# Performance work log

Measured on AMD Instinct MI355X. Metric: run time of the kernel, lower is better.

## Reference

```python
import jax, jax.numpy as jnp
import numpy as np

NUM_ANCHORS = 32
MAX_DIST = 3
DDE_ROUNDS = 2
DDE_REV_ROUNDS = 2
PE_ANCHOR_DIM = 16


def setup_inputs() -> dict:
    key = jax.random.key(0)
    ks = jax.random.split(key, 20)
    N, Ntext, NT, E, R, D, H = 20000, 19500, 500, 200000, 500, 256, 256
    PE = DDE_ROUNDS + DDE_REV_ROUNDS + PE_ANCHOR_DIM + 3
    s = 0.02
    return {
        "h_ids": jax.random.randint(ks[0], (E,), 0, N),
        "r_ids": jax.random.randint(ks[1], (E,), 0, R),
        "t_ids": jax.random.randint(ks[2], (E,), 0, N),
        "q_emb": jax.random.normal(ks[3], (D,), jnp.float32),
        "entity_embs": jax.random.normal(ks[4], (Ntext, D), jnp.float32),
        "relation_embs": jax.random.normal(ks[5], (R, D), jnp.float32),
        "topic_entity_ids": jax.random.randint(ks[6], (4,), 0, N),
        "num_entities": N,
        "num_non_text_entities": NT,
        "non_text_emb": jax.random.normal(ks[7], (1, D)) * s,
        "dist_emb": jax.random.normal(ks[8], (MAX_DIST + 2, PE_ANCHOR_DIM)) * s,
        "W_enc": jax.random.normal(ks[9], (D + PE, H)) * s,
        "b_enc": jnp.zeros((H,)),
        "gnn_W_msg": jax.random.normal(ks[10], (2, H + D, H)) * s,
        "gnn_W_gate": jax.random.normal(ks[11], (2, 2 * H, H)) * s,
        "gnn_W_upd": jax.random.normal(ks[12], (2, H, H)) * s,
        "W_out": jax.random.normal(ks[13], (H, D)) * s,
        "scorer_W1": jax.random.normal(ks[14], (4 * D + 4, H)) * s,
        "scorer_b1": jnp.zeros((H,)),
        "scorer_W2": jax.random.normal(ks[15], (H, 1)) * s,
        "scorer_b2": jnp.zeros((1,)),
    }


def reference(h_ids, r_ids, t_ids, q_emb, entity_embs, relation_embs,
              topic_entity_ids, num_entities, num_non_text_entities,
              non_text_emb, dist_emb, W_enc, b_enc,
              gnn_W_msg, gnn_W_gate, gnn_W_upd, W_out,
              scorer_W1, scorer_b1, scorer_W2, scorer_b2):
    N = num_entities
    D = q_emb.shape[0]
    E = h_ids.shape[0]
    # assemble all entity embeddings (text + broadcast non-text)
    all_emb = jnp.concatenate(
        [entity_embs, jnp.broadcast_to(non_text_emb, (num_non_text_entities, D))], axis=0)
    # anchor triple selection: question-conditioned triple scores, top-k
    qe = all_emb @ q_emb            # [N]
    qr = relation_embs @ q_emb      # [R]
    tri_score = qe[h_ids] + qr[r_ids] + qe[t_ids]  # [E]
    anchor_scores, anchor_idx = jax.lax.top_k(tri_score, NUM_ANCHORS)
    # topic DDE positional encoding (mean-aggregated label propagation)
    topic = jnp.zeros((N,), all_emb.dtype).at[topic_entity_ids].set(1.0)
    deg_t = jnp.maximum(jnp.zeros((N,)).at[t_ids].add(1.0), 1.0)
    deg_h = jnp.maximum(jnp.zeros((N,)).at[h_ids].add(1.0), 1.0)
    cols = []
    s = topic
    for _ in range(DDE_ROUNDS):
        s = jnp.zeros((N,)).at[t_ids].add(s[h_ids]) / deg_t
        cols.append(s)
    s = topic
    for _ in range(DDE_REV_ROUNDS):
        s = jnp.zeros((N,)).at[h_ids].add(s[t_ids]) / deg_h
        cols.append(s)
    pe_topic = jnp.stack(cols, axis=1)  # [N, 4]
    # anchor proximity PE: bounded BFS distance, embedded
    anchor_mask = (jnp.zeros((N,)).at[h_ids[anchor_idx]].set(1.0)
                   .at[t_ids[anchor_idx]].set(1.0))
    FAR = float(MAX_DIST + 1)
    dist = jnp.where(anchor_mask > 0, 0.0, FAR)
    for _ in range(MAX_DIST):
        c1 = jnp.full((N,), FAR).at[t_ids].min(dist[h_ids] + 1.0)
        c2 = jnp.full((N,), FAR).at[h_ids].min(dist[t_ids] + 1.0)
        dist = jnp.minimum(dist, jnp.minimum(c1, c2))
    pe_anchor = dist_emb[dist.astype(jnp.int32)]  # [N, 16]
    # path indicators (topic flag, anchor-endpoint flag, subgraph mask = full graph)
    path_ind = jnp.stack([topic, anchor_mask, jnp.ones((N,))], axis=1)
    pe_full = jnp.concatenate([pe_topic, pe_anchor, path_ind], axis=1)  # [N, 23]
    # gated GNN refine over the (full) anchor subgraph
    h = jax.nn.relu(jnp.concatenate([all_emb, pe_full], axis=1) @ W_enc + b_enc)
    rel_e = relation_embs[r_ids]  # [E, D]
    for l in range(gnn_W_msg.shape[0]):
        msg = jax.nn.relu(jnp.concatenate([h[h_ids], rel_e], axis=1) @ gnn_W_msg[l])
        agg = jnp.zeros_like(h).at[t_ids].add(msg)
        gate = jax.nn.sigmoid(jnp.concatenate([h, agg], axis=1) @ gnn_W_gate[l])
        h = h + gate * jnp.tanh(agg @ gnn_W_upd[l])
    h_final = h @ W_out  # back to emb_dim, assembled over all entities
    # scalar triple features
    is_anchor = jnp.zeros((E,)).at[anchor_idx].set(1.0)
    a_score = jnp.zeros((E,)).at[anchor_idx].set(jax.lax.stop_gradient(anchor_scores))
    scalar_feats = jnp.stack([is_anchor, a_score, topic[h_ids], topic[t_ids]], axis=1)
    # triple scorer MLP
    feats = jnp.concatenate([
        jnp.broadcast_to(q_emb, (E, D)), h_final[h_ids], rel_e,
        h_final[t_ids], scalar_feats], axis=1)  # [E, 4D+4]
    hid = jax.nn.relu(feats @ scorer_W1 + scorer_b1)
    return (hid @ scorer_W2 + scorer_b2)[:, 0]
```

## Files before the change

### kernel.cpp

```cpp
#include <hip/hip_runtime.h>
#include <math.h>

#define CDIV(a,b) (((a)+(b)-1)/(b))

typedef short short8 __attribute__((ext_vector_type(8)));
typedef float f32x4  __attribute__((ext_vector_type(4)));
typedef unsigned short u16;

__device__ __forceinline__ float warp_sum(float v){
  #pragma unroll
  for (int o=32;o;o>>=1) v += __shfl_down(v,o);
  return v;
}
__device__ __forceinline__ int warp_min(int v){
  #pragma unroll
  for (int o=32;o;o>>=1) v = min(v,__shfl_down(v,o));
  return v;
}
__device__ __forceinline__ u16 f2bf(float f){
  unsigned u = __float_as_uint(f);
  unsigned r = 0x7fffu + ((u>>16)&1u);
  return (u16)((u + r)>>16);
}
__device__ __forceinline__ float bl(u16 v){ return __uint_as_float(((unsigned)v)<<16); }

__global__ __launch_bounds__(256)
void k_rowdot_all(const float* __restrict__ ent, const float* __restrict__ nontext,
                  const float* __restrict__ q, float* __restrict__ qe,
                  int N, int Ntext,
                  const float* __restrict__ rel, float* __restrict__ qr, int R, int nb1){
  int wid = threadIdx.x>>6, lane = threadIdx.x&63;
  const float* src; float* dst; int row;
  if ((int)blockIdx.x < nb1){
    row = blockIdx.x*4 + wid; if (row >= N) return;
    src = (row < Ntext) ? (ent + (size_t)row*256) : nontext;
    dst = qe;
  } else {
    row = (blockIdx.x-nb1)*4 + wid; if (row >= R) return;
    src = rel + (size_t)row*256;
    dst = qr;
  }
  float4 a = *(const float4*)(src + lane*4);
  float4 b = *(const float4*)(q + lane*4);
  float s = a.x*b.x + a.y*b.y + a.z*b.z + a.w*b.w;
  s = warp_sum(s);
  if (!lane) dst[row] = s;
}

__global__ __launch_bounds__(256)
void k_tri(const int* __restrict__ h, const int* __restrict__ r,
           const int* __restrict__ t, const float* __restrict__ qe,
           const float* __restrict__ qr, float* __restrict__ tri,
           float* __restrict__ bmax, int* __restrict__ degh, int* __restrict__ degi, int E){
  __shared__ float red[256];
  int e = blockIdx.x*256 + threadIdx.x;
  float v = -INFINITY;
  if (e < E){
    int hh=h[e], rr=r[e], tt=t[e];
    v = qe[hh] + qr[rr] + qe[tt];
    tri[e] = v;
    atomicAdd(&degh[hh], 1);
    atomicAdd(&degi[tt], 1);
  }
  red[threadIdx.x]=v; __syncthreads();
  for (int s=128;s;s>>=1){ if ((int)threadIdx.x<s) red[threadIdx.x]=fmaxf(red[threadIdx.x],red[threadIdx.x+s]); __syncthreads(); }
  if (!threadIdx.x) bmax[blockIdx.x]=red[0];
}

__global__ __launch_bounds__(64)
void k_thresh(const float* __restrict__ bmax, float* __restrict__ thrT, int nb){
  int lane = threadIdx.x;
  float m = -INFINITY;
  for (int i=lane; i<nb; i+=64) m = fmaxf(m, bmax[i]);
  for (int it=0; it<32; it++){
    float bv = m; int bln = lane;
    #pragma unroll
    for (int o=32;o;o>>=1){
      float ov = __shfl_down(bv,o);
      int   ol = __shfl_down(bln,o);
      if (ov>bv){ bv=ov; bln=ol; }
    }
    float mv = __shfl(bv,0);
    int   wl = __shfl(bln,0);
    if (lane==wl) m = -INFINITY;
    if (it==31 && lane==0) thrT[0]=mv;
  }
}

__global__ void k_compact(const float* __restrict__ tri, const float* __restrict__ thrT,
                          int* __restrict__ cnt, int* __restrict__ ci, float* __restrict__ cv, int E){
  int e = blockIdx.x*256 + threadIdx.x; if (e>=E) return;
  float v = tri[e];
  if (v >= thrT[0]){
    int p = atomicAdd(cnt, 1);
    ci[p]=e; cv[p]=v;
  }
}

__global__ __launch_bounds__(64)
void k_final32(const int* __restrict__ ci, const float* __restrict__ cv, const int* __restrict__ cnt,
               int* __restrict__ ai, float* __restrict__ as,
               const int* __restrict__ h_ids, const int* __restrict__ t_ids,
               const int* __restrict__ topicId, int nTopic,
               float* __restrict__ topic, float* __restrict__ amask){
  int lane = threadIdx.x;
  int C = *cnt; if (C > 1024) C = 1024;
  int nIter = CDIV(C,64);
  unsigned selMask = 0;
  int myai=0; float myas=0.f;
  for (int it=0; it<32; it++){
    float bv=-INFINITY; int bi=0x7fffffff; int bj=-1;
    for (int j=0;j<nIter;j++){
      int p = lane + j*64;
      if (p < C && !((selMask>>j)&1u)){
        float v = cv[p]; int idx = ci[p];
        if (v>bv || (v==bv && idx<bi)){ bv=v; bi=idx; bj=j; }
      }
    }
    int bln = lane;
    #pragma unroll
    for (int o=32;o;o>>=1){
      float ov=__shfl_down(bv,o); int oi=__shfl_down(bi,o);
      int   oj=__shfl_down(bj,o); int ol=__shfl_down(bln,o);
      if (ov>bv || (ov==bv && oi<bi)){ bv=ov; bi=oi; bj=oj; bln=ol; }
    }
    float wv=__shfl(bv,0); int wi=__shfl(bi,0);
    int   wj=__shfl(bj,0); int wl=__shfl(bln,0);
    if (lane==wl) selMask |= (1u<<wj);
    if (lane==it){ myai=wi; myas=wv; }
  }
  if (lane<32){
    ai[lane]=myai; as[lane]=myas;
    int e = myai;
    amask[h_ids[e]]=1.f;
    amask[t_ids[e]]=1.f;
  }
  if (lane<nTopic) topic[topicId[lane]]=1.f;
}

__global__ void k_scan1(const int* __restrict__ degT, const int* __restrict__ degH,
                        int* __restrict__ offsT, int* __restrict__ offsH,
                        int* __restrict__ bsum, int N, int nb){
  __shared__ int s[256];
  int which = (int)blockIdx.x >= nb;
  int b = which ? blockIdx.x - nb : blockIdx.x;
  const int* deg = which ? degH : degT;
  int* offs = which ? offsH : offsT;
  int i = b*256 + threadIdx.x;
  int v = (i<N) ? deg[i] : 0;
  s[threadIdx.x] = v; __syncthreads();
  #pragma unroll
  for (int o=1;o<256;o<<=1){
    int add = (threadIdx.x>=(unsigned)o) ? s[threadIdx.x-o] : 0; __syncthreads();
    s[threadIdx.x] += add; __syncthreads();
  }
  if (i<N) offs[i] = s[threadIdx.x] - v;
  if (threadIdx.x==255) bsum[blockIdx.x] = s[255];
}
__global__ void k_scan2two(int* __restrict__ bsum, int nb){
  __shared__ int s[256];
  int t=threadIdx.x;
  int half = t>>7, idx = t&127;
  int v = (idx<nb)? bsum[half*nb+idx] : 0;
  s[t]=v; __syncthreads();
  #pragma unroll
  for (int o=1;o<128;o<<=1){ int add=(idx>=o)?s[t-o]:0; __syncthreads(); s[t]+=add; __syncthreads(); }
  if (idx<nb) bsum[half*nb+idx] = s[t]-v;
}
__global__ void k_scan3(int* __restrict__ offsT, int* __restrict__ offsH,
                        const int* __restrict__ bsum,
                        int* __restrict__ curT, int* __restrict__ curH, int N, int nb){
  int which = (int)blockIdx.x >= nb;
  int b = which ? blockIdx.x - nb : blockIdx.x;
  int i = b*256+threadIdx.x; if (i>=N) return;
  int* offs = which ? offsH : offsT;
  int* cur  = which ? curH  : curT;
  int o = offs[i] + bsum[blockIdx.x];
  offs[i]=o; cur[i]=o;
}
__global__ void k_place(const int* __restrict__ h, const int* __restrict__ r,
                        const int* __restrict__ t,
                        int* __restrict__ curT, int* __restrict__ curH,
                        int4* __restrict__ ehr4, int* __restrict__ etH, int E){
  int e = blockIdx.x*256+threadIdx.x; if (e>=E) return;
  int hh=h[e], tt=t[e];
  int pos = atomicAdd(&curT[tt], 1);
  ehr4[pos] = make_int4(hh, r[e], e, 0);
  int posh = atomicAdd(&curH[hh], 1);
  etH[posh] = tt;
}

__global__ __launch_bounds__(256)
void k_dde2(const int* __restrict__ offsT, const int* __restrict__ degT, const int4* __restrict__ ehr4,
            const int* __restrict__ offsH, const int* __restrict__ degH, const int* __restrict__ etH,
            const float* __restrict__ s0, const float* __restrict__ s1,
            float* __restrict__ sn0, float* __restrict__ sn1,
            float* __restrict__ pe4, int c0, int c1,
            const float* __restrict__ amask, int* __restrict__ dist0, int N){
  int wid=threadIdx.x>>6, lane=threadIdx.x&63;
  int i = blockIdx.x*4+wid; if (i>=N) return;
  int dir = blockIdx.y;
  const int* offs = dir ? offsH : offsT;
  const int* deg  = dir ? degH  : degT;
  const float* s  = dir ? s1 : s0;
  float* sn       = dir ? sn1 : sn0;
  int col         = dir ? c1 : c0;
  int start=offs[i], cnt=deg[i];
  float a=0.f;
  if (dir){
    for (int k=lane;k<cnt;k+=64) a += s[etH[start+k]];
  } else {
    for (int k=lane;k<cnt;k+=64) a += s[ehr4[start+k].x];
  }
  a = warp_sum(a);
  if (!lane){
    float v = a / fmaxf((float)cnt,1.f);
    if (sn) sn[i]=v;
    pe4[i*4+col]=v;
    if (dist0 && !dir) dist0[i] = (amask[i]>0.f)?0:4;
  }
}

__global__ __launch_bounds__(256)
void k_bfs_g(const int* __restrict__ offsT, const int* __restrict__ degT, const int4* __restrict__ ehr4,
             const int* __restrict__ offsH, const int* __restrict__ degH, const int* __restrict__ etH,
             const int* __restrict__ din, int* __restrict__ dout, int N){
  int wid=threadIdx.x>>6, lane=threadIdx.x&63;
  int i = blockIdx.x*4+wid; if (i>=N) return;
  int sT=offsT[i], cT=degT[i];
  int sH=offsH[i], cH=degH[i];
  int best = 4;
  for (int k=lane;k<cT;k+=64) best = min(best, din[ehr4[sT+k].x]+1);
  for (int k=lane;k<cH;k+=64) best = min(best, din[etH[sH+k]]+1);
  best = warp_min(best);
  if (!lane) dout[i] = min(din[i], best);
}

__global__ void k_smalls(const float* __restrict__ dist_e, const float* __restrict__ W_enc,
                         float* __restrict__ distW,
                         const float* __restrict__ nontext, float* __restrict__ encnt,
                         const float* __restrict__ q, const float* __restrict__ W1,
                         const float* __restrict__ b1, float* __restrict__ bias2){
  int b = blockIdx.x, j = threadIdx.x;
  if (b < 5){
    const float* Wpe = W_enc + (256+4)*256;
    float s=0.f;
    #pragma unroll
    for (int p=0;p<16;p++) s += dist_e[b*16+p]*Wpe[p*256+j];
    distW[b*256+j]=s;
  } else if (b == 5){
    float s=0.f;
    for (int k=0;k<256;k++) s += nontext[k]*W_enc[k*256+j];
    encnt[j]=s;
  } else {
    float s=b1[j];
    for (int k=0;k<256;k++) s += q[k]*W1[k*256+j];
    bias2[j]=s;
  }
}

__global__ __launch_bounds__(64)
void k_packall(const float* __restrict__ W_enc, const float* __restrict__ W_msg,
               const float* __restrict__ W_gate, const float* __restrict__ W_upd,
               const float* __restrict__ W1, u16* __restrict__ pbAll){
  int f = blockIdx.x, lane = threadIdx.x;
  int tgt, fid, nt16;
  if      (f < 128) { tgt=0; fid=f;      nt16=16; }
  else if (f < 256) { tgt=1; fid=f-128;  nt16=16; }
  else if (f < 384) { tgt=2; fid=f-256;  nt16=16; }
  else if (f < 896) { tgt=3; fid=f-384;  nt16=32; }
  else if (f < 1408){ tgt=4; fid=f-896;  nt16=32; }
  else if (f < 1792){ tgt=5; fid=f-1408; nt16=48; }
  else              { tgt=6; fid=f-1792; nt16=32; }
  int ks = fid/nt16, nt = fid%nt16;
  int kb = ks*32 + 8*(lane>>4);
  int n  = nt*16 + (lane&15);
  u16 v[8];
  #pragma unroll
  for (int i=0;i<8;i++){
    int k = kb+i;
    float x;
    if (tgt==0) x = W_enc[(size_t)k*256+n];
    else if (tgt==1) x = W_msg[(size_t)k*256+n];
    else if (tgt==2) x = W_msg[(size_t)(512+k)*256+n];
    else if (tgt==3 || tgt==4){
      const float* Wg = W_gate + (tgt==4 ? (size_t)512*256 : 0);
      const float* Wu = W_upd  + (tgt==4 ? (size_t)256*256 : 0);
      int blk = n>>4, c = ((blk>>1)<<4) | (n&15);
      if ((blk&1)==0) x = Wg[(size_t)k*256+c];
      else            x = (k<256) ? 0.f : Wu[(size_t)(k-256)*256+c];
    }
    else if (tgt==5){
      if (n<256)      x = W_msg[(size_t)(256+k)*256+n];
      else if (n<512) x = W_msg[(size_t)(768+k)*256+(n-256)];
      else            x = W1[(size_t)(512+k)*256+(n-512)];
    } else {
      if (n<256) x = W1[(size_t)(256+k)*256+n];
      else       x = W1[(size_t)(768+k)*256+(n-256)];
    }
    v[i]=f2bf(x);
  }
  *(uint4*)(pbAll + ((size_t)f*64+lane)*8) = *(uint4*)v;
}

__global__ __launch_bounds__(64)
void k_packf32(const float* __restrict__ W, u16* __restrict__ Bp){
  int f = blockIdx.x, lane = threadIdx.x;
  int ks = f/32, nt = f%32;
  int kb = ks*32 + 8*(lane>>4);
  int n  = nt*16 + (lane&15);
  u16 v[8];
  #pragma unroll
  for (int i=0;i<8;i++) v[i] = f2bf(W[(size_t)(kb+i)*512 + n]);
  *(uint4*)(Bp + ((size_t)f*64+lane)*8) = *(uint4*)v;
}

template<int NCOLS, int CT, int MODE, bool AF32, int MR>
__global__ __launch_bounds__(256)
void k_bgemm(const float* __restrict__ A1f, const u16* __restrict__ A2a,
             const u16* __restrict__ A2b, int K1,
             const u16* __restrict__ Bp, void* __restrict__ Cout,
             const float* __restrict__ xb, const float* __restrict__ W_enc,
             const float* __restrict__ pe4, const int* __restrict__ dist,
             const float* __restrict__ topic, const float* __restrict__ amask,
             const float* __restrict__ distW,
             int M, int K)
{
  constexpr int NT16 = NCOLS/16;
  constexpr int CPB  = NCOLS/CT;
  constexpr int NREP = CPB/32;
  const int tid  = threadIdx.x;
  const int lane = tid & 63;
  const int w    = tid >> 6;
  const int wr   = w >> 1, wc = w & 1;
  const int ct   = blockIdx.y;
  const int row0 = (blockIdx.x*2 + wr)*(16*MR);
  const int lrow = lane & 15;
  const int kc   = lane >> 4;
  int arow[MR];
  #pragma unroll
  for (int m=0;m<MR;m++){
    int rr = row0 + m*16 + lrow;
    arow[m] = (rr >= M) ? M-1 : rr;
  }

  f32x4 acc[MR][NREP];
  #pragma unroll
  for (int m=0;m<MR;m++)
    #pragma unroll
    for (int n=0;n<NREP;n++) acc[m][n] = (f32x4){0.f,0.f,0.f,0.f};

  const int ksteps = K/32;
  const int fcolBase = ct*(CPB/16) + wc*NREP;

  auto do_step = [&](short8* af, int ks){
    const u16* bp = Bp + ((size_t)(ks*NT16 + fcolBase)*64 + lane)*8;
    #pragma unroll
    for (int n=0;n<NREP;n++){
      short8 bf = *(const short8*)(bp + (size_t)n*64*8);
      #pragma unroll
      for (int m=0;m<MR;m++)
        acc[m][n] = __builtin_amdgcn_mfma_f32_16x16x32_bf16(af[m], bf, acc[m][n], 0, 0, 0);
    }
  };

  if (AF32){
    for (int ks=0; ks<ksteps; ks++){
      short8 af[MR];
      #pragma unroll
      for (int m=0;m<MR;m++){
        const float* ap = A1f + (size_t)arow[m]*256 + ks*32 + kc*8;
        float4 a0 = *(const float4*)ap;
        float4 a1 = *(const float4*)(ap+4);
        af[m][0]=(short)f2bf(a0.x); af[m][1]=(short)f2bf(a0.y); af[m][2]=(short)f2bf(a0.z); af[m][3]=(short)f2bf(a0.w);
        af[m][4]=(short)f2bf(a1.x); af[m][5]=(short)f2bf(a1.y); af[m][6]=(short)f2bf(a1.z); af[m][7]=(short)f2bf(a1.w);
      }
      do_step(af, ks);
    }
  } else {
    int s1 = K1>>5; if (s1 > ksteps) s1 = ksteps;
    for (int ks=0; ks<s1; ks++){
      short8 af[MR];
      #pragma unroll
      for (int m=0;m<MR;m++)
        af[m] = *(const short8*)(A2a + (size_t)arow[m]*256 + ks*32 + kc*8);
      do_step(af, ks);
    }
    for (int ks=s1; ks<ksteps; ks++){
      short8 af[MR];
      #pragma unroll
      for (int m=0;m<MR;m++)
        af[m] = *(const short8*)(A2b + (size_t)arow[m]*256 + (ks-s1)*32 + kc*8);
      do_step(af, ks);
    }
  }

  #pragma unroll
  for (int m=0;m<MR;m++){
    #pragma unroll
    for (int r=0;r<4;r++){
      int orow = row0 + m*16 + 4*kc + r;
      if (orow >= M) continue;
      if (MODE==0 || MODE==1){
        #pragma unroll
        for (int n=0;n<NREP;n++){
          int col = ct*CPB + wc*(CPB/2) + n*16 + lrow;
          float v = acc[m][n][r];
          if (MODE==0) ((float*)Cout)[(size_t)orow*NCOLS + col] = v;
          else         ((u16*)Cout)[(size_t)orow*NCOLS + col] = f2bf(v);
        }
      } else if (MODE==5){
        float tp = topic[orow];
        #pragma unroll
        for (int n=0;n<NREP;n++){
          int col = ct*CPB + wc*(CPB/2) + n*16 + lrow;
          float v = acc[m][n][r] + tp*xb[col];
          ((u16*)Cout)[(size_t)orow*NCOLS + col] = f2bf(v);
        }
      } else if (MODE==6){
        #pragma unroll
        for (int n=0;n<NREP;n++){
          int col = ct*CPB + wc*(CPB/2) + n*16 + lrow;
          float v = acc[m][n][r];
          if (col >= 512) v += xb[col-512];
          ((u16*)Cout)[(size_t)orow*NCOLS + col] = f2bf(v);
        }
      } else if (MODE==3){
        float p0=pe4[orow*4+0], p1=pe4[orow*4+1], p2=pe4[orow*4+2], p3=pe4[orow*4+3];
        int dd=dist[orow];
        float tp=topic[orow], am=amask[orow];
        const float* Wpe = W_enc + 256*256;
        #pragma unroll
        for (int n=0;n<NREP;n++){
          int col = ct*CPB + wc*(CPB/2) + n*16 + lrow;
          float v = acc[m][n][r];
          v += xb[col] + Wpe[22*256+col]
             + p0*Wpe[col] + p1*Wpe[256+col] + p2*Wpe[512+col] + p3*Wpe[768+col]
             + distW[dd*256+col] + tp*Wpe[20*256+col] + am*Wpe[21*256+col];
          ((u16*)Cout)[(size_t)orow*256 + col] = f2bf(fmaxf(v, 0.f));
        }
      } else {
        #pragma unroll
        for (int k=0;k<NREP/2;k++){
          int col = (ct*(CPB/32) + wc*(CPB/64) + k)*16 + lrow;
          size_t idx = (size_t)orow*256 + col;
          float g = 1.f/(1.f+expf(-acc[m][2*k][r]));
          float u = tanhf(acc[m][2*k+1][r]);
          float v = bl(A2a[idx]) + g*u;
          ((u16*)Cout)[idx] = f2bf(v);
        }
      }
    }
  }
}

__global__ __launch_bounds__(256)
void k_encnt_fill(const float* __restrict__ encnt, const float* __restrict__ b_enc,
                  const float* __restrict__ W_enc, const float* __restrict__ pe4,
                  const int* __restrict__ dist, const float* __restrict__ topic,
                  const float* __restrict__ amask, const float* __restrict__ distW,
                  u16* __restrict__ hB, int Ntext){
  int i = Ntext + blockIdx.x, j = threadIdx.x;
  const float* Wpe = W_enc + 256*256;
  float p0=pe4[i*4+0], p1=pe4[i*4+1], p2=pe4[i*4+2], p3=pe4[i*4+3];
  int d = dist[i];
  float tp = topic[i], am = amask[i];
  float v = encnt[j] + b_enc[j] + Wpe[22*256+j]
          + p0*Wpe[j] + p1*Wpe[256+j] + p2*Wpe[512+j] + p3*Wpe[768+j]
          + distW[d*256+j] + tp*Wpe[20*256+j] + am*Wpe[21*256+j];
  hB[(size_t)i*256+j] = f2bf(fmaxf(v, 0.f));
}

__global__ __launch_bounds__(256)
void k_agg(const int* __restrict__ offs, const int* __restrict__ degi,
           const int4* __restrict__ ehr4,
           const u16* __restrict__ hm, const u16* __restrict__ relC, int colOff,
           u16* __restrict__ agg, int N){
  int wid = threadIdx.x>>6, lane = threadIdx.x&63;
  int i = blockIdx.x*4 + wid; if (i>=N) return;
  int start = offs[i], cnt = degi[i];
  int c4 = lane*4;
  float a0=0.f,a1=0.f,a2=0.f,a3=0.f;
  int k=0;
  for (; k+1<cnt; k+=2){
    int4 h0 = ehr4[start+k];
    int4 h1 = ehr4[start+k+1];
    uint2 ua0 = *(const uint2*)(hm + (size_t)h0.x*256 + c4);
    uint2 ub0 = *(const uint2*)(relC + (size_t)h0.y*768 + colOff + c4);
    uint2 ua1 = *(const uint2*)(hm + (size_t)h1.x*256 + c4);
    uint2 ub1 = *(const uint2*)(relC + (size_t)h1.y*768 + colOff + c4);
    a0 += fmaxf(bl((u16)(ua0.x&0xffff))+bl((u16)(ub0.x&0xffff)),0.f)
        + fmaxf(bl((u16)(ua1.x&0xffff))+bl((u16)(ub1.x&0xffff)),0.f);
    a1 += fmaxf(bl((u16)(ua0.x>>16))  +bl((u16)(ub0.x>>16)),  0.f)
        + fmaxf(bl((u16)(ua1.x>>16))  +bl((u16)(ub1.x>>16)),  0.f);
    a2 += fmaxf(bl((u16)(ua0.y&0xffff))+bl((u16)(ub0.y&0xffff)),0.f)
        + fmaxf(bl((u16)(ua1.y&0xffff))+bl((u16)(ub1.y&0xffff)),0.f);
    a3 += fmaxf(bl((u16)(ua0.y>>16))  +bl((u16)(ub0.y>>16)),  0.f)
        + fmaxf(bl((u16)(ua1.y>>16))  +bl((u16)(ub1.y>>16)),  0.f);
  }
  if (k<cnt){
    int4 hr = ehr4[start+k];
    uint2 ua = *(const uint2*)(hm + (size_t)hr.x*256 + c4);
    uint2 ub = *(const uint2*)(relC + (size_t)hr.y*768 + colOff + c4);
    a0 += fmaxf(bl((u16)(ua.x&0xffff))+bl((u16)(ub.x&0xffff)),0.f);
    a1 += fmaxf(bl((u16)(ua.x>>16))  +bl((u16)(ub.x>>16)),  0.f);
    a2 += fmaxf(bl((u16)(ua.y&0xffff))+bl((u16)(ub.y&0xffff)),0.f);
    a3 += fmaxf(bl((u16)(ua.y>>16))  +bl((u16)(ub.y>>16)),  0.f);
  }
  uint2 o;
  o.x = (unsigned)f2bf(a0) | ((unsigned)f2bf(a1)<<16);
  o.y = (unsigned)f2bf(a2) | ((unsigned)f2bf(a3)<<16);
  *(uint2*)(agg + (size_t)i*256 + c4) = o;
}

__global__ __launch_bounds__(256)
void k_score(const int* __restrict__ offs, const int* __restrict__ degi,
             const int4* __restrict__ ehr4,
             const u16* __restrict__ UHT, const u16* __restrict__ relC,
             const float* __restrict__ W2,
             const float* __restrict__ b2, float* __restrict__ out, int N){
  int wid = threadIdx.x>>6, lane = threadIdx.x&63;
  int i = blockIdx.x*4 + wid; if (i>=N) return;
  int start = offs[i], cnt = degi[i];
  if (!cnt) return;
  int c = lane*4;
  uint2 ud = *(const uint2*)(UHT + (size_t)i*512 + 256 + c);
  float b0 = bl((u16)(ud.x&0xffff)), b1v = bl((u16)(ud.x>>16));
  float b2v= bl((u16)(ud.y&0xffff)), b3  = bl((u16)(ud.y>>16));
  float4 w = *(const float4*)(W2 + c);
  float bout = b2[0];
  int k=0;
  for (; k+1<cnt; k+=2){
    int4 e0 = ehr4[start+k];
    int4 e1 = ehr4[start+k+1];
    uint2 ua0 = *(const uint2*)(UHT + (size_t)e0.x*512 + c);
    uint2 ub0 = *(const uint2*)(relC + (size_t)e0.y*768 + 512 + c);
    uint2 ua1 = *(const uint2*)(UHT + (size_t)e1.x*512 + c);
    uint2 ub1 = *(const uint2*)(relC + (size_t)e1.y*768 + 512 + c);
    float p = fmaxf(b0 + bl((u16)(ua0.x&0xffff)) + bl((u16)(ub0.x&0xffff)),0.f)*w.x
            + fmaxf(b1v+ bl((u16)(ua0.x>>16))    + bl((u16)(ub0.x>>16)),  0.f)*w.y
            + fmaxf(b2v+ bl((u16)(ua0.y&0xffff)) + bl((u16)(ub0.y&0xffff)),0.f)*w.z
            + fmaxf(b3 + bl((u16)(ua0.y>>16))    + bl((u16)(ub0.y>>16)),  0.f)*w.w;
    float q = fmaxf(b0 + bl((u16)(ua1.x&0xffff)) + bl((u16)(ub1.x&0xffff)),0.f)*w.x
            + fmaxf(b1v+ bl((u16)(ua1.x>>16))    + bl((u16)(ub1.x>>16)),  0.f)*w.y
            + fmaxf(b2v+ bl((u16)(ua1.y&0xffff)) + bl((u16)(ub1.y&0xffff)),0.f)*w.z
            + fmaxf(b3 + bl((u16)(ua1.y>>16))    + bl((u16)(ub1.y>>16)),  0.f)*w.w;
    p = warp_sum(p);
    q = warp_sum(q);
    if (!lane){ out[e0.z] = p + bout; out[e1.z] = q + bout; }
  }
  if (k<cnt){
    int4 e0 = ehr4[start+k];
    uint2 ua = *(const uint2*)(UHT + (size_t)e0.x*512 + c);
    uint2 ub = *(const uint2*)(relC + (size_t)e0.y*768 + 512 + c);
    float p = fmaxf(b0 + bl((u16)(ua.x&0xffff)) + bl((u16)(ub.x&0xffff)),0.f)*w.x
            + fmaxf(b1v+ bl((u16)(ua.x>>16))    + bl((u16)(ub.x>>16)),  0.f)*w.y
            + fmaxf(b2v+ bl((u16)(ua.y&0xffff)) + bl((u16)(ub.y&0xffff)),0.f)*w.z
            + fmaxf(b3 + bl((u16)(ua.y>>16))    + bl((u16)(ub.y>>16)),  0.f)*w.w;
    p = warp_sum(p);
    if (!lane) out[e0.z] = p + bout;
  }
}

__global__ __launch_bounds__(256)
void k_patch(const int* __restrict__ ai, const float* __restrict__ as,
             const int* __restrict__ h_ids, const int* __restrict__ r_ids, const int* __restrict__ t_ids,
             const u16* __restrict__ UHT, const u16* __restrict__ relC,
             const float* __restrict__ W1s, const float* __restrict__ W2,
             const float* __restrict__ b2, float* __restrict__ out){
  int wid = threadIdx.x>>6, lane = threadIdx.x&63;
  int k = blockIdx.x*4 + wid; if (k>=32) return;
  int e = ai[k];
  int h=h_ids[e], r=r_ids[e], t=t_ids[e];
  float aS = as[k];
  int c = lane*4;
  uint2 ua = *(const uint2*)(UHT + (size_t)h*512 + c);
  uint2 ud = *(const uint2*)(UHT + (size_t)t*512 + 256 + c);
  uint2 ub = *(const uint2*)(relC + (size_t)r*768 + 512 + c);
  float4 w0 = *(const float4*)(W1s + 0*256 + c);
  float4 w1 = *(const float4*)(W1s + 1*256 + c);
  float4 acc;
  acc.x = bl((u16)(ua.x&0xffff))+bl((u16)(ub.x&0xffff))+bl((u16)(ud.x&0xffff)) + w0.x + aS*w1.x;
  acc.y = bl((u16)(ua.x>>16))  +bl((u16)(ub.x>>16))  +bl((u16)(ud.x>>16))   + w0.y + aS*w1.y;
  acc.z = bl((u16)(ua.y&0xffff))+bl((u16)(ub.y&0xffff))+bl((u16)(ud.y&0xffff)) + w0.z + aS*w1.z;
  acc.w = bl((u16)(ua.y>>16))  +bl((u16)(ub.y>>16))  +bl((u16)(ud.y>>16))   + w0.w + aS*w1.w;
  acc.x=fmaxf(acc.x,0.f); acc.y=fmaxf(acc.y,0.f); acc.z=fmaxf(acc.z,0.f); acc.w=fmaxf(acc.w,0.f);
  float4 w = *(const float4*)(W2 + c);
  float p = acc.x*w.x + acc.y*w.y + acc.z*w.z + acc.w*w.w;
  p = warp_sum(p);
  if (!lane) out[e] = p + b2[0];
}

extern "C" void kernel_launch(void* const* d_in, const int* in_sizes, int n_in,
                              void* d_out, int out_size, void* d_ws, size_t ws_size,
                              hipStream_t stream)
{
  const int*   h_ids   = (const int*)d_in[0];
  const int*   r_ids   = (const int*)d_in[1];
  const int*   t_ids   = (const int*)d_in[2];
  const float* q       = (const float*)d_in[3];
  const float* ent     = (const float*)d_in[4];
  const float* rel     = (const float*)d_in[5];
  const int*   topicId = (const int*)d_in[6];
  const float* nontext = (const float*)d_in[9];
  const float* dist_e  = (const float*)d_in[10];
  const float* W_enc   = (const float*)d_in[11];
  const float* b_enc   = (const float*)d_in[12];
  const float* W_msg   = (const float*)d_in[13];
  const float* W_gate  = (const float*)d_in[14];
  const float* W_upd   = (const float*)d_in[15];
  const float* W_out   = (const float*)d_in[16];
  const float* W1      = (const float*)d_in[17];
  const float* b1      = (const float*)d_in[18];
  const float* W2      = (const float*)d_in[19];
  const float* b2      = (const float*)d_in[20];
  float* out = (float*)d_out;

  const int E = in_sizes[0];
  const int Ntext = in_sizes[4]/256;
  const int R = in_sizes[5]/256;
  const int NT = 500;
  const int N = Ntext + NT;
  const int nTopic = in_sizes[6];
  const int BIGK1 = 1<<28;

  char* ws = (char*)d_ws;
  size_t off = 0;
  auto alloc = [&](size_t bytes)->void*{
    size_t o = (off + 255) & ~(size_t)255;
    off = o + bytes;
    return (void*)(ws + o);
  };
  u16*   hB1   = (u16*)  alloc((size_t)N*256*2);
  u16*   hB2   = (u16*)  alloc((size_t)N*256*2);
  u16*   hmB   = (u16*)  alloc((size_t)N*256*2);
  u16*   aggB  = (u16*)  alloc((size_t)N*256*2);
  u16*   relC  = (u16*)  alloc((size_t)R*768*2);
  u16*   UHT   = (u16*)  alloc((size_t)N*512*2);
  float* WcombF= (float*)alloc((size_t)256*512*4);
  u16*   pbWcomb=(u16*)  alloc((size_t)256*512*2);
  float* qe    = (float*)alloc((size_t)N*4);
  float* qr    = (float*)alloc((size_t)R*4);
  float* tri   = (float*)alloc((size_t)E*4);
  float* bmax  = (float*)alloc(1024*4);
  float* thrT  = (float*)alloc(4);
  int*   ci    = (int*)  alloc((size_t)E*4);
  float* cv    = (float*)alloc((size_t)E*4);
  int*   ai    = (int*)  alloc(32*4);
  float* as    = (float*)alloc(32*4);
  float* pe4   = (float*)alloc((size_t)N*16);
  int*   dA    = (int*)  alloc((size_t)N*4);
  int*   dB    = (int*)  alloc((size_t)N*4);
  float* distW = (float*)alloc(5*256*4);
  float* encnt = (float*)alloc(256*4);
  float* bias2 = (float*)alloc(256*4);
  int*   offsT = (int*)  alloc((size_t)N*4);
  int*   offsH = (int*)  alloc((size_t)N*4);
  int*   bsum  = (int*)  alloc(256*4);
  int*   curT  = (int*)  alloc((size_t)N*4);
  int*   curH  = (int*)  alloc((size_t)N*4);
  int4*  ehr4  = (int4*) alloc((size_t)E*16);
  int*   etH   = (int*)  alloc((size_t)E*4);
  float* sA    = (float*)alloc((size_t)N*4);
  float* sB    = (float*)alloc((size_t)N*4);
  u16*   pbAll = (u16*)  alloc((size_t)2048*512*2);
  int*   cnt   = (int*)  alloc(4);
  float* topic = (float*)alloc((size_t)N*4);
  float* amask = (float*)alloc((size_t)N*4);
  int*   deghI = (int*)  alloc((size_t)N*4);
  int*   degiI = (int*)  alloc((size_t)N*4);
  (void)ws_size; (void)n_in; (void)out_size;

  size_t zbytes = (char*)(degiI + N) - (char*)cnt;
  hipMemsetAsync(cnt, 0, zbytes, stream);

  u16* pbWenc = pbAll + (size_t)0*512;
  u16* pbWmT0 = pbAll + (size_t)128*512;
  u16* pbWmT1 = pbAll + (size_t)256*512;
  u16* pbGU0  = pbAll + (size_t)384*512;
  u16* pbGU1  = pbAll + (size_t)896*512;
  u16* pbRelC = pbAll + (size_t)1408*512;
  u16* pbW1ht = pbAll + (size_t)1792*512;

  const float* tW = W1 + (size_t)(1024+2)*256;

  k_packall<<<2048,64,0,stream>>>(W_enc, W_msg, W_gate, W_upd, W1, pbAll);
  k_bgemm<512,1,0,true,1><<<dim3(8,1),256,0,stream>>>(W_out, nullptr, nullptr, BIGK1, pbW1ht, WcombF,
      nullptr,nullptr,nullptr,nullptr,nullptr,nullptr,nullptr, 256, 256);
  k_packf32<<<256,64,0,stream>>>(WcombF, pbWcomb);

  int nb1 = CDIV(N,4);
  k_rowdot_all<<<nb1+CDIV(R,4),256,0,stream>>>(ent, nontext, q, qe, N, Ntext, rel, qr, R, nb1);
  int nbE = CDIV(E,256);
  k_tri<<<nbE,256,0,stream>>>(h_ids, r_ids, t_ids, qe, qr, tri, bmax, deghI, degiI, E);
  k_thresh<<<1,64,0,stream>>>(bmax, thrT, nbE);
  k_compact<<<nbE,256,0,stream>>>(tri, thrT, cnt, ci, cv, E);
  k_final32<<<1,64,0,stream>>>(ci, cv, cnt, ai, as, h_ids, t_ids, topicId, nTopic, topic, amask);

  int nb = CDIV(N,256);
  k_scan1<<<2*nb,256,0,stream>>>(degiI, deghI, offsT, offsH, bsum, N, nb);
  k_scan2two<<<1,256,0,stream>>>(bsum, nb);
  k_scan3<<<2*nb,256,0,stream>>>(offsT, offsH, bsum, curT, curH, N, nb);
  k_place<<<nbE,256,0,stream>>>(h_ids, r_ids, t_ids, curT, curH, ehr4, etH, E);

  int nbN4 = CDIV(N,4);
  k_dde2<<<dim3(nbN4,2),256,0,stream>>>(offsT, degiI, ehr4, offsH, deghI, etH,
      topic, topic, sB, sA, pe4, 0, 2, nullptr, nullptr, N);
  k_dde2<<<dim3(nbN4,2),256,0,stream>>>(offsT, degiI, ehr4, offsH, deghI, etH,
      sB, sA, nullptr, nullptr, pe4, 1, 3, amask, dA, N);

  k_bfs_g<<<nbN4,256,0,stream>>>(offsT, degiI, ehr4, offsH, deghI, etH, dA, dB, N);
  k_bfs_g<<<nbN4,256,0,stream>>>(offsT, degiI, ehr4, offsH, deghI, etH, dB, dA, N);
  k_bfs_g<<<nbN4,256,0,stream>>>(offsT, degiI, ehr4, offsH, deghI, etH, dA, dB, N);

  k_smalls<<<7,256,0,stream>>>(dist_e, W_enc, distW, nontext, encnt, q, W1, b1, bias2);

  k_bgemm<768,6,6,true,1><<<dim3(CDIV(R,32),6),256,0,stream>>>(rel, nullptr, nullptr, BIGK1, pbRelC, relC,
      bias2,nullptr,nullptr,nullptr,nullptr,nullptr,nullptr, R, 256);

  k_bgemm<256,2,3,true,2><<<dim3(CDIV(Ntext,64),2),256,0,stream>>>(ent, nullptr, nullptr, BIGK1, pbWenc, hB1,
      b_enc, W_enc, pe4, dB, topic, amask, distW, Ntext, 256);
  k_encnt_fill<<<N-Ntext,256,0,stream>>>(encnt, b_enc, W_enc, pe4, dB, topic, amask, distW, hB1, Ntext);

  for (int l=0;l<2;l++){
    const u16* pT = l ? pbWmT1 : pbWmT0;
    const u16* pGU = l ? pbGU1 : pbGU0;
    u16* hinB  = l ? hB2 : hB1;
    u16* houtB = l ? hB1 : hB2;
    k_bgemm<256,2,1,false,2><<<dim3(CDIV(N,64),2),256,0,stream>>>(nullptr, hinB, nullptr, BIGK1, pT, hmB,
        nullptr,nullptr,nullptr,nullptr,nullptr,nullptr,nullptr, N, 256);
    k_agg<<<CDIV(N,4),256,0,stream>>>(offsT, degiI, ehr4, hmB, relC, l*256, aggB, N);
    k_bgemm<512,2,4,false,2><<<dim3(CDIV(N,64),2),256,0,stream>>>(nullptr, hinB, aggB, 256, pGU, houtB,
        nullptr,nullptr,nullptr,nullptr,nullptr,nullptr,nullptr, N, 512);
  }

  k_bgemm<512,2,5,false,2><<<dim3(CDIV(N,64),2),256,0,stream>>>(nullptr, hB1, nullptr, BIGK1, pbWcomb, UHT,
      tW,nullptr,nullptr,nullptr,topic,nullptr,nullptr, N, 256);

  k_score<<<CDIV(N,4),256,0,stream>>>(offsT, degiI, ehr4, UHT, relC, W2, b2, out, N);
  k_patch<<<8,256,0,stream>>>(ai, as, h_ids, r_ids, t_ids, UHT, relC,
                              W1+(size_t)1024*256, W2, b2, out);
}
```

Baseline: 425.9 us.

## Unroll edge gathers by four and split GEMM columns across more blocks

The aggregation and scoring kernels now issue four edge-index loads and their row gathers before doing any arithmetic, instead of two. This puts more independent memory requests in flight per wave to hide gather latency. Separately, the GEMM launches raise the column-split template parameter and grid y-dimension (2→4, 1→8), so there are more blocks with narrower column slices each. That adds parallelism for the N≈20k row GEMMs but re-reads the A tiles more often and raises register pressure in the unrolled loops.

```diff
diff --git a/kernel.cpp b/kernel.cpp
--- a/kernel.cpp
+++ b/kernel.cpp
@@ -482,23 +482,24 @@
   int c4 = lane*4;
   float a0=0.f,a1=0.f,a2=0.f,a3=0.f;
   int k=0;
-  for (; k+1<cnt; k+=2){
-    int4 h0 = ehr4[start+k];
-    int4 h1 = ehr4[start+k+1];
-    uint2 ua0 = *(const uint2*)(hm + (size_t)h0.x*256 + c4);
-    uint2 ub0 = *(const uint2*)(relC + (size_t)h0.y*768 + colOff + c4);
-    uint2 ua1 = *(const uint2*)(hm + (size_t)h1.x*256 + c4);
-    uint2 ub1 = *(const uint2*)(relC + (size_t)h1.y*768 + colOff + c4);
-    a0 += fmaxf(bl((u16)(ua0.x&0xffff))+bl((u16)(ub0.x&0xffff)),0.f)
-        + fmaxf(bl((u16)(ua1.x&0xffff))+bl((u16)(ub1.x&0xffff)),0.f);
-    a1 += fmaxf(bl((u16)(ua0.x>>16))  +bl((u16)(ub0.x>>16)),  0.f)
-        + fmaxf(bl((u16)(ua1.x>>16))  +bl((u16)(ub1.x>>16)),  0.f);
-    a2 += fmaxf(bl((u16)(ua0.y&0xffff))+bl((u16)(ub0.y&0xffff)),0.f)
-        + fmaxf(bl((u16)(ua1.y&0xffff))+bl((u16)(ub1.y&0xffff)),0.f);
-    a3 += fmaxf(bl((u16)(ua0.y>>16))  +bl((u16)(ub0.y>>16)),  0.f)
-        + fmaxf(bl((u16)(ua1.y>>16))  +bl((u16)(ub1.y>>16)),  0.f);
-  }
-  if (k<cnt){
+  for (; k+3<cnt; k+=4){
+    int4 hr[4]; uint2 ua[4], ub[4];
+    #pragma unroll
+    for (int j=0;j<4;j++) hr[j] = ehr4[start+k+j];
+    #pragma unroll
+    for (int j=0;j<4;j++){
+      ua[j] = *(const uint2*)(hm + (size_t)hr[j].x*256 + c4);
+      ub[j] = *(const uint2*)(relC + (size_t)hr[j].y*768 + colOff + c4);
+    }
+    #pragma unroll
+    for (int j=0;j<4;j++){
+      a0 += fmaxf(bl((u16)(ua[j].x&0xffff))+bl((u16)(ub[j].x&0xffff)),0.f);
+      a1 += fmaxf(bl((u16)(ua[j].x>>16))  +bl((u16)(ub[j].x>>16)),  0.f);
+      a2 += fmaxf(bl((u16)(ua[j].y&0xffff))+bl((u16)(ub[j].y&0xffff)),0.f);
+      a3 += fmaxf(bl((u16)(ua[j].y>>16))  +bl((u16)(ub[j].y>>16)),  0.f);
+    }
+  }
+  for (; k<cnt; k++){
     int4 hr = ehr4[start+k];
     uint2 ua = *(const uint2*)(hm + (size_t)hr.x*256 + c4);
     uint2 ub = *(const uint2*)(relC + (size_t)hr.y*768 + colOff + c4);
@@ -530,26 +531,31 @@
   float4 w = *(const float4*)(W2 + c);
   float bout = b2[0];
   int k=0;
-  for (; k+1<cnt; k+=2){
-    int4 e0 = ehr4[start+k];
-    int4 e1 = ehr4[start+k+1];
-    uint2 ua0 = *(const uint2*)(UHT + (size_t)e0.x*512 + c);
-    uint2 ub0 = *(const uint2*)(relC + (size_t)e0.y*768 + 512 + c);
-    uint2 ua1 = *(const uint2*)(UHT + (size_t)e1.x*512 + c);
-    uint2 ub1 = *(const uint2*)(relC + (size_t)e1.y*768 + 512 + c);
-    float p = fmaxf(b0 + bl((u16)(ua0.x&0xffff)) + bl((u16)(ub0.x&0xffff)),0.f)*w.x
-            + fmaxf(b1v+ bl((u16)(ua0.x>>16))    + bl((u16)(ub0.x>>16)),  0.f)*w.y
-            + fmaxf(b2v+ bl((u16)(ua0.y&0xffff)) + bl((u16)(ub0.y&0xffff)),0.f)*w.z
-            + fmaxf(b3 + bl((u16)(ua0.y>>16))    + bl((u16)(ub0.y>>16)),  0.f)*w.w;
-    float q = fmaxf(b0 + bl((u16)(ua1.x&0xffff)) + bl((u16)(ub1.x&0xffff)),0.f)*w.x
-            + fmaxf(b1v+ bl((u16)(ua1.x>>16))    + bl((u16)(ub1.x>>16)),  0.f)*w.y
-            + fmaxf(b2v+ bl((u16)(ua1.y&0xffff)) + bl((u16)(ub1.y&0xffff)),0.f)*w.z
-            + fmaxf(b3 + bl((u16)(ua1.y>>16))    + bl((u16)(ub1.y>>16)),  0.f)*w.w;
-    p = warp_sum(p);
-    q = warp_sum(q);
-    if (!lane){ out[e0.z] = p + bout; out[e1.z] = q + bout; }
-  }
-  if (k<cnt){
+  for (; k+3<cnt; k+=4){
+    int4 e[4]; uint2 ua[4], ub[4];
+    #pragma unroll
+    for (int j=0;j<4;j++) e[j] = ehr4[start+k+j];
+    #pragma unroll
+    for (int j=0;j<4;j++){
+      ua[j] = *(const uint2*)(UHT + (size_t)e[j].x*512 + c);
+      ub[j] = *(const uint2*)(relC + (size_t)e[j].y*768 + 512 + c);
+    }
+    float p[4];
+    #pragma unroll
+    for (int j=0;j<4;j++){
+      p[j] = fmaxf(b0 + bl((u16)(ua[j].x&0xffff)) + bl((u16)(ub[j].x&0xffff)),0.f)*w.x
+           + fmaxf(b1v+ bl((u16)(ua[j].x>>16))    + bl((u16)(ub[j].x>>16)),  0.f)*w.y
+           + fmaxf(b2v+ bl((u16)(ua[j].y&0xffff)) + bl((u16)(ub[j].y&0xffff)),0.f)*w.z
+           + fmaxf(b3 + bl((u16)(ua[j].y>>16))    + bl((u16)(ub[j].y>>16)),  0.f)*w.w;
+    }
+    #pragma unroll
+    for (int j=0;j<4;j++) p[j] = warp_sum(p[j]);
+    if (!lane){
+      #pragma unroll
+      for (int j=0;j<4;j++) out[e[j].z] = p[j] + bout;
+    }
+  }
+  for (; k<cnt; k++){
     int4 e0 = ehr4[start+k];
     uint2 ua = *(const uint2*)(UHT + (size_t)e0.x*512 + c);
     uint2 ub = *(const uint2*)(relC + (size_t)e0.y*768 + 512 + c);
@@ -685,7 +691,7 @@
   const float* tW = W1 + (size_t)(1024+2)*256;
 
   k_packall<<<2048,64,0,stream>>>(W_enc, W_msg, W_gate, W_upd, W1, pbAll);
-  k_bgemm<512,1,0,true,1><<<dim3(8,1),256,0,stream>>>(W_out, nullptr, nullptr, BIGK1, pbW1ht, WcombF,
+  k_bgemm<512,8,0,true,1><<<dim3(8,8),256,0,stream>>>(W_out, nullptr, nullptr, BIGK1, pbW1ht, WcombF,
       nullptr,nullptr,nullptr,nullptr,nullptr,nullptr,nullptr, 256, 256);
   k_packf32<<<256,64,0,stream>>>(WcombF, pbWcomb);
 
@@ -718,7 +724,7 @@
   k_bgemm<768,6,6,true,1><<<dim3(CDIV(R,32),6),256,0,stream>>>(rel, nullptr, nullptr, BIGK1, pbRelC, relC,
       bias2,nullptr,nullptr,nullptr,nullptr,nullptr,nullptr, R, 256);
 
-  k_bgemm<256,2,3,true,2><<<dim3(CDIV(Ntext,64),2),256,0,stream>>>(ent, nullptr, nullptr, BIGK1, pbWenc, hB1,
+  k_bgemm<256,4,3,true,2><<<dim3(CDIV(Ntext,64),4),256,0,stream>>>(ent, nullptr, nullptr, BIGK1, pbWenc, hB1,
       b_enc, W_enc, pe4, dB, topic, amask, distW, Ntext, 256);
   k_encnt_fill<<<N-Ntext,256,0,stream>>>(encnt, b_enc, W_enc, pe4, dB, topic, amask, distW, hB1, Ntext);
 
@@ -727,14 +733,14 @@
     const u16* pGU = l ? pbGU1 : pbGU0;
     u16* hinB  = l ? hB2 : hB1;
     u16* houtB = l ? hB1 : hB2;
-    k_bgemm<256,2,1,false,2><<<dim3(CDIV(N,64),2),256,0,stream>>>(nullptr, hinB, nullptr, BIGK1, pT, hmB,
+    k_bgemm<256,4,1,false,2><<<dim3(CDIV(N,64),4),256,0,stream>>>(nullptr, hinB, nullptr, BIGK1, pT, hmB,
         nullptr,nullptr,nullptr,nullptr,nullptr,nullptr,nullptr, N, 256);
     k_agg<<<CDIV(N,4),256,0,stream>>>(offsT, degiI, ehr4, hmB, relC, l*256, aggB, N);
-    k_bgemm<512,2,4,false,2><<<dim3(CDIV(N,64),2),256,0,stream>>>(nullptr, hinB, aggB, 256, pGU, houtB,
+    k_bgemm<512,4,4,false,2><<<dim3(CDIV(N,64),4),256,0,stream>>>(nullptr, hinB, aggB, 256, pGU, houtB,
         nullptr,nullptr,nullptr,nullptr,nullptr,nullptr,nullptr, N, 512);
   }
 
-  k_bgemm<512,2,5,false,2><<<dim3(CDIV(N,64),2),256,0,stream>>>(nullptr, hB1, nullptr, BIGK1, pbWcomb, UHT,
+  k_bgemm<512,4,5,false,2><<<dim3(CDIV(N,64),4),256,0,stream>>>(nullptr, hB1, nullptr, BIGK1, pbWcomb, UHT,
       tW,nullptr,nullptr,nullptr,topic,nullptr,nullptr, N, 256);
 
   k_score<<<CDIV(N,4),256,0,stream>>>(offsT, degiI, ehr4, UHT, relC, W2, b2, out, N);
```

Result: faster. 402.5 us (-5.5%).
